# Kernel optimization log

Measured on AMD Instinct MI355X. Metric: run time of the kernel, lower is better.

## Reference

```python
import jax, jax.numpy as jnp
import numpy as np

NUM_CLASSES = 80
NUM_ANCHORS = 5
ANCHORS = np.array([1.3221, 1.73145, 3.19275, 4.00944, 5.05587, 8.09892,
                    9.47112, 4.84053, 11.2364, 10.0071], dtype=np.float32).reshape(NUM_ANCHORS, 2)
COORD_SCALE = 1.0
NOOBJECT_SCALE = 1.0
OBJECT_SCALE = 5.0
CLASS_SCALE = 1.0
SIL_THRESH = 0.6
MAX_T = 50  # max ground-truth boxes per image
NB, NH, NW = 32, 38, 38


def bbox_iou(b1, b2):
    """IoU for center-format boxes (..., 4) = (cx, cy, w, h); broadcastable.
    Matches darknet bbox_ious with x1y1x2y2=False (zero IoU if no overlap)."""
    mx = jnp.minimum(b1[..., 0] - b1[..., 2] / 2, b2[..., 0] - b2[..., 2] / 2)
    Mx = jnp.maximum(b1[..., 0] + b1[..., 2] / 2, b2[..., 0] + b2[..., 2] / 2)
    my = jnp.minimum(b1[..., 1] - b1[..., 3] / 2, b2[..., 1] - b2[..., 3] / 2)
    My = jnp.maximum(b1[..., 1] + b1[..., 3] / 2, b2[..., 1] + b2[..., 3] / 2)
    cw = b1[..., 2] + b2[..., 2] - (Mx - mx)
    ch = b1[..., 3] + b2[..., 3] - (My - my)
    inter = jnp.where((cw > 0) & (ch > 0), cw * ch, 0.0)
    union = b1[..., 2] * b1[..., 3] + b2[..., 2] * b2[..., 3] - inter
    return inter / jnp.maximum(union, 1e-12)


def setup_inputs() -> dict:
    key = jax.random.key(0)
    k1, k2, k3 = jax.random.split(key, 3)
    output = jax.random.normal(k1, (NB, NUM_ANCHORS * (5 + NUM_CLASSES), NH, NW), dtype=jnp.float32)
    # target rows: 50 boxes x (cls, x, y, w, h), normalized coords in (0,1)
    target = jax.random.uniform(k2, (NB, MAX_T * 5), dtype=jnp.float32, minval=0.02, maxval=0.98)
    features = jax.random.normal(k3, (NB, 512, NH, NW), dtype=jnp.float32)
    return {"output": output, "target": target, "features": features}


def _region_loss(output, target):
    nB, _, nH, nW = output.shape
    nA, nC = NUM_ANCHORS, NUM_CLASSES
    anchors = jnp.asarray(ANCHORS)
    sg = jax.lax.stop_gradient

    out5 = output.reshape(nB, nA, 5 + nC, nH, nW)
    x = jax.nn.sigmoid(out5[:, :, 0])
    y = jax.nn.sigmoid(out5[:, :, 1])
    w = out5[:, :, 2]
    h = out5[:, :, 3]
    conf = jax.nn.sigmoid(out5[:, :, 4])
    cls = jnp.transpose(out5[:, :, 5:], (0, 1, 3, 4, 2))  # [nB,nA,nH,nW,nC]

    # predicted boxes in grid units (detached, as pred_boxes uses .data in torch)
    grid_x = jnp.arange(nW, dtype=output.dtype)
    grid_y = jnp.arange(nH, dtype=output.dtype)
    px = sg(x) + grid_x[None, None, None, :]
    py = sg(y) + grid_y[None, None, :, None]
    pw = jnp.exp(sg(w)) * anchors[None, :, 0, None, None]
    ph = jnp.exp(sg(h)) * anchors[None, :, 1, None, None]
    pred_boxes = jnp.stack([px, py, pw, ph], axis=-1)  # [nB,nA,nH,nW,4]

    tgt = sg(target).reshape(nB, MAX_T, 5)
    gx = tgt[..., 1] * nW
    gy = tgt[..., 2] * nH
    gw = tgt[..., 3] * nW
    gh = tgt[..., 4] * nH
    # original loop breaks at first target x == 0 -> valid prefix mask
    valid = jnp.cumprod((tgt[..., 1] != 0).astype(jnp.int32), axis=1).astype(bool)

    # ---- conf_mask silencing: max IoU of every predicted box vs any GT ----
    gt_boxes = jnp.stack([gx, gy, gw, gh], axis=-1)  # [nB,50,4]
    pb_flat = pred_boxes.reshape(nB, 1, nA * nH * nW, 4)
    ious = bbox_iou(gt_boxes[:, :, None, :], pb_flat)  # [nB,50,nA*nH*nW]
    max_iou = jnp.where(valid[:, :, None], ious, 0.0).max(axis=1).reshape(nB, nA, nH, nW)
    conf_mask = jnp.where(max_iou > SIL_THRESH, 0.0, NOOBJECT_SCALE).astype(output.dtype)

    # ---- seen < 12800 warm-up branch (self.seen = 0, anchor_step = 2) ----
    shp = (nB, nA, nH, nW)
    tx = jnp.full(shp, 0.5, output.dtype)
    ty = jnp.full(shp, 0.5, output.dtype)
    tw = jnp.zeros(shp, output.dtype)
    th = jnp.zeros(shp, output.dtype)
    coord_mask = jnp.ones(shp, output.dtype)
    cls_mask = jnp.zeros(shp, output.dtype)
    tconf = jnp.zeros(shp, output.dtype)
    tcls = jnp.zeros(shp, jnp.int32)

    # ---- best anchor per GT (IoU of wh-only boxes; argmax keeps first max,
    #      matching the strict '>' update in the loop) ----
    zeros = jnp.zeros_like(gw)
    gt_wh = jnp.stack([zeros, zeros, gw, gh], axis=-1)[:, :, None, :]  # [nB,50,1,4]
    anc_wh = jnp.concatenate([jnp.zeros_like(anchors), anchors], axis=-1)[None, None]  # [1,1,nA,4]
    best_n = jnp.argmax(bbox_iou(gt_wh, anc_wh), axis=-1)  # [nB,50]

    gi = jnp.clip(jnp.floor(gx).astype(jnp.int32), 0, nW - 1)
    gj = jnp.clip(jnp.floor(gy).astype(jnp.int32), 0, nH - 1)

    b_idx = jnp.arange(nB)[:, None]
    pbox = pred_boxes[b_idx, best_n, gj, gi]  # [nB,50,4]
    iou_gt = bbox_iou(gt_boxes, pbox)  # [nB,50]

    tx_val = gx - gi.astype(output.dtype)
    ty_val = gy - gj.astype(output.dtype)
    tw_val = jnp.log(jnp.maximum(gw, 1e-12) / anchors[best_n, 0])
    th_val = jnp.log(jnp.maximum(gh, 1e-12) / anchors[best_n, 1])
    cls_val = tgt[..., 0].astype(jnp.int32)

    bi = jnp.arange(nB)

    def step(carry, t):
        coord_m, conf_m, cls_m, tx, ty, tw, th, tconf, tcls = carry
        bn = best_n[:, t]
        j = gj[:, t]
        i = gi[:, t]
        v = valid[:, t]

        def upd(arr, val):
            # indices are distinct within one step (one GT per batch element)
            old = arr[bi, bn, j, i]
            return arr.at[bi, bn, j, i].set(jnp.where(v, val, old))

        coord_m = upd(coord_m, 1.0)
        cls_m = upd(cls_m, 1.0)
        conf_m = upd(conf_m, OBJECT_SCALE)
        tx = upd(tx, tx_val[:, t])
        ty = upd(ty, ty_val[:, t])
        tw = upd(tw, tw_val[:, t])
        th = upd(th, th_val[:, t])
        tconf = upd(tconf, iou_gt[:, t])
        tcls = upd(tcls, cls_val[:, t])
        return (coord_m, conf_m, cls_m, tx, ty, tw, th, tconf, tcls), None

    init = (coord_mask, conf_mask, cls_mask, tx, ty, tw, th, tconf, tcls)
    (coord_mask, conf_mask, cls_mask, tx, ty, tw, th, tconf, tcls), _ = jax.lax.scan(
        step, init, jnp.arange(MAX_T))

    conf_mask = jnp.sqrt(conf_mask)

    loss_x = COORD_SCALE * jnp.sum((x * coord_mask - tx * coord_mask) ** 2) / 2.0
    loss_y = COORD_SCALE * jnp.sum((y * coord_mask - ty * coord_mask) ** 2) / 2.0
    loss_w = COORD_SCALE * jnp.sum((w * coord_mask - tw * coord_mask) ** 2) / 2.0
    loss_h = COORD_SCALE * jnp.sum((h * coord_mask - th * coord_mask) ** 2) / 2.0
    loss_conf = jnp.sum((conf * conf_mask - tconf * conf_mask) ** 2) / 2.0

    # sum-reduced cross entropy over cells where cls_mask == 1
    logp = jax.nn.log_softmax(cls, axis=-1)
    picked = jnp.take_along_axis(logp, tcls[..., None], axis=-1)[..., 0]
    loss_cls = -CLASS_SCALE * jnp.sum(cls_mask * picked)

    return loss_x + loss_y + loss_w + loss_h + loss_conf + loss_cls


def reference(output, target, features):
    # `features` feeds the truncated adversarial-defense tail of the original
    # forward; the detection region loss below is the complete surviving math.
    return _region_loss(output, target)
```

## Files before the change

### kernel.cpp

```cpp
#include <hip/hip_runtime.h>
#include <math.h>

#define NB 32
#define NA 5
#define NC 80
#define NH 38
#define NW 38
#define MAXT 50
#define CELLS (NH * NW)
#define CH (5 + NC)
#define REC_STRIDE 12
#define PREP_THREADS 256
#define NWAVES (PREP_THREADS / 64)

__device__ __forceinline__ float sigmoidf_(float v) {
    return 1.0f / (1.0f + expf(-v));
}

__device__ __forceinline__ float bbox_iou_(float ax, float ay, float aw, float ah,
                                           float bx, float by, float bw, float bh) {
    float mx = fminf(ax - aw * 0.5f, bx - bw * 0.5f);
    float Mx = fmaxf(ax + aw * 0.5f, bx + bw * 0.5f);
    float my = fminf(ay - ah * 0.5f, by - bh * 0.5f);
    float My = fmaxf(ay + ah * 0.5f, by + bh * 0.5f);
    float cw = aw + bw - (Mx - mx);
    float ch = ah + bh - (My - my);
    float inter = (cw > 0.0f && ch > 0.0f) ? cw * ch : 0.0f;
    float uni = aw * ah + bw * bh - inter;
    return inter / fmaxf(uni, 1e-12f);
}

__device__ __constant__ float c_anchors[10] = {
    1.3221f, 1.73145f, 3.19275f, 4.00944f, 5.05587f,
    8.09892f, 9.47112f, 4.84053f, 11.2364f, 10.0071f};

#define CLS_PART_OFF (NB * MAXT * REC_STRIDE)

__global__ void prep_gt_kernel(const float* __restrict__ out,
                               const float* __restrict__ tgt,
                               float* __restrict__ ws,
                               float* __restrict__ loss_out,
                               int out_size) {
    const int b = blockIdx.x;
    const int tid = threadIdx.x;
    const int wid = tid >> 6;
    const int lane = tid & 63;
    const int t = tid;

    if (b == 0) {
        for (int i = tid; i < out_size; i += PREP_THREADS) loss_out[i] = 0.0f;
    }

    __shared__ int s_nz[64];
    __shared__ int s_key[64];
    __shared__ int s_winner[MAXT];
    __shared__ int s_off[MAXT];
    __shared__ int s_cls[MAXT];
    __shared__ float s_cpart[NWAVES];

    float t0 = 0.f, t1 = 0.f, gx = 0.f, gy = 0.f, gw = 0.f, gh = 0.f;
    if (t < MAXT) {
        const float* tp = tgt + (long)b * (MAXT * 5) + t * 5;
        t0 = tp[0];
        t1 = tp[1];
        gx = t1 * NW;
        gy = tp[2] * NH;
        gw = tp[3] * NW;
        gh = tp[4] * NH;
    }
    if (t < 64) s_nz[t] = (t < MAXT) ? (t1 != 0.0f ? 1 : 0) : 1;
    __syncthreads();

    int key = -1;
    if (t < MAXT) {
        bool valid = true;
        for (int u = 0; u <= t; ++u)
            if (!s_nz[u]) { valid = false; break; }

        int bn = 0;
        float best = -1.0f;
        for (int a = 0; a < NA; ++a) {
            float aw = c_anchors[2 * a], ah = c_anchors[2 * a + 1];
            float inter = fminf(gw, aw) * fminf(gh, ah);
            float uni = gw * gh + aw * ah - inter;
            float iou = inter / fmaxf(uni, 1e-12f);
            if (iou > best) { best = iou; bn = a; }
        }
        int gi = (int)floorf(gx);
        gi = gi < 0 ? 0 : (gi > NW - 1 ? NW - 1 : gi);
        int gj = (int)floorf(gy);
        gj = gj < 0 ? 0 : (gj > NH - 1 ? NH - 1 : gj);

        long base = (((long)b * NA + bn) * CH) * CELLS + gj * NW + gi;
        float xr = out[base];
        float yr = out[base + CELLS];
        float wr = out[base + 2 * CELLS];
        float hr = out[base + 3 * CELLS];
        float px = sigmoidf_(xr) + (float)gi;
        float py = sigmoidf_(yr) + (float)gj;
        float pw = expf(wr) * c_anchors[2 * bn];
        float ph = expf(hr) * c_anchors[2 * bn + 1];
        float iou_gt = bbox_iou_(gx, gy, gw, gh, px, py, pw, ph);
        float txv = gx - (float)gi;
        float tyv = gy - (float)gj;
        float twv = logf(fmaxf(gw, 1e-12f) / c_anchors[2 * bn]);
        float thv = logf(fmaxf(gh, 1e-12f) / c_anchors[2 * bn + 1]);

        key = valid ? (bn * CELLS + gj * NW + gi) : -1;

        float* r = ws + ((long)b * MAXT + t) * REC_STRIDE;
        r[0] = gx; r[1] = gy; r[2] = gw; r[3] = gh;
        r[4] = valid ? 1.0f : 0.0f;
        r[5] = (float)key;
        r[6] = txv; r[7] = tyv; r[8] = twv; r[9] = thv;
        r[10] = iou_gt;
        r[11] = 0.0f;

        int cls = (int)t0;
        cls = cls < 0 ? 0 : (cls > NC - 1 ? NC - 1 : cls);
        s_cls[t] = cls;
        s_off[t] = (bn * CH + 5) * CELLS + gj * NW + gi;
    }
    if (t < 64) s_key[t] = key;
    __syncthreads();

    if (t < MAXT) {
        bool winner = (key >= 0);
        if (winner) {
            for (int u = t + 1; u < MAXT; ++u)
                if (s_key[u] == key) { winner = false; break; }
        }
        s_winner[t] = winner ? 1 : 0;
    }
    __syncthreads();

    const float* ob = out + (long)b * NA * CH * CELLS;
    float closs = 0.0f;
    for (int rt = wid; rt < MAXT; rt += NWAVES) {
        if (!s_winner[rt]) continue;
        const float* cp = ob + s_off[rt];
        float v0 = cp[(long)lane * CELLS];
        float v1 = (lane < NC - 64) ? cp[(long)(64 + lane) * CELLS] : -INFINITY;
        float m = fmaxf(v0, v1);
        for (int off = 32; off > 0; off >>= 1)
            m = fmaxf(m, __shfl_down(m, off));
        m = __shfl(m, 0);
        float e = expf(v0 - m) + ((lane < NC - 64) ? expf(v1 - m) : 0.0f);
        for (int off = 32; off > 0; off >>= 1)
            e += __shfl_down(e, off);
        if (lane == 0) {
            float lse = m + logf(e);
            closs += lse - cp[(long)s_cls[rt] * CELLS];
        }
    }
    if (lane == 0) s_cpart[wid] = closs;
    __syncthreads();
    if (tid == 0) {
        float s = 0.0f;
        for (int w = 0; w < NWAVES; ++w) s += s_cpart[w];
        ws[CLS_PART_OFF + b] = s;
    }
}

__global__ void cell_loss_kernel(const float* __restrict__ out,
                                 const float* __restrict__ ws,
                                 float* __restrict__ loss) {
    const int b = blockIdx.y;
    const int idx = blockIdx.x * blockDim.x + threadIdx.x;

    __shared__ float sr[MAXT][REC_STRIDE];
    for (int k = threadIdx.x; k < MAXT * REC_STRIDE; k += blockDim.x)
        ((float*)sr)[k] = ws[(long)b * MAXT * REC_STRIDE + k];
    __syncthreads();

    float cell = 0.0f;
    if (idx < NA * CELLS) {
        int a = idx / CELLS;
        int r = idx - a * CELLS;
        int j = r / NW;
        int i = r - j * NW;

        long base = (((long)b * NA + a) * CH) * CELLS + r;
        float xr = out[base];
        float yr = out[base + CELLS];
        float wr = out[base + 2 * CELLS];
        float hr = out[base + 3 * CELLS];
        float cr = out[base + 4 * CELLS];

        float sx = sigmoidf_(xr);
        float sy = sigmoidf_(yr);
        float sc = sigmoidf_(cr);
        float px = sx + (float)i;
        float py = sy + (float)j;
        float pw = expf(wr) * c_anchors[2 * a];
        float ph = expf(hr) * c_anchors[2 * a + 1];

        float mykey = (float)(a * CELLS + r);
        float max_iou = 0.0f;
        int m = -1;
        #pragma unroll 5
        for (int t = 0; t < MAXT; ++t) {
            if (sr[t][4] != 0.0f) {
                float iou = bbox_iou_(sr[t][0], sr[t][1], sr[t][2], sr[t][3],
                                      px, py, pw, ph);
                max_iou = fmaxf(max_iou, iou);
                if (sr[t][5] == mykey) m = t;
            }
        }

        float tx = 0.5f, ty = 0.5f, tw = 0.0f, th = 0.0f, tconf = 0.0f;
        float cscale = (max_iou > 0.6f) ? 0.0f : 1.0f;
        if (m >= 0) {
            tx = sr[m][6]; ty = sr[m][7]; tw = sr[m][8]; th = sr[m][9];
            tconf = sr[m][10];
            cscale = 5.0f;
        }
        float dx = sx - tx, dy = sy - ty, dw = wr - tw, dh = hr - th, dc = sc - tconf;
        cell = 0.5f * (dx * dx + dy * dy + dw * dw + dh * dh) + 0.5f * cscale * dc * dc;
    }

    float v = cell;
    for (int off = 32; off > 0; off >>= 1) v += __shfl_down(v, off);
    __shared__ float swave[4];
    int wid = threadIdx.x >> 6;
    int lane = threadIdx.x & 63;
    if (lane == 0) swave[wid] = v;
    __syncthreads();
    if (threadIdx.x == 0) {
        float s = swave[0] + swave[1] + swave[2] + swave[3];
        if (blockIdx.x == 0) s += ws[CLS_PART_OFF + b];
        atomicAdd(loss, s);
    }
}

extern "C" void kernel_launch(void* const* d_in, const int* in_sizes, int n_in,
                              void* d_out, int out_size, void* d_ws, size_t ws_size,
                              hipStream_t stream) {
    const float* output = (const float*)d_in[0];
    const float* target = (const float*)d_in[1];
    float* loss = (float*)d_out;
    float* ws = (float*)d_ws;

    prep_gt_kernel<<<NB, PREP_THREADS, 0, stream>>>(output, target, ws, loss, out_size);
    const int cells = NA * CELLS;
    dim3 grid((cells + 255) / 256, NB);
    cell_loss_kernel<<<grid, 256, 0, stream>>>(output, ws, loss);
}
```

Before: 206.2 us.

## Fuse GT prep and per-cell loss into one kernel with redundant per-block prep

Merges the ground-truth preparation kernel and the per-cell loss kernel into a single kernel launched over 8 slices per batch image. Each block recomputes the GT records in shared memory instead of passing them through a global workspace, then grid-strides over its slice of cells and shares the class-loss rows across slices. This removes the dependency between the two kernels and the workspace round trip. The cost is that GT prep is repeated 8 times per image, there is a separate tiny zeroing launch, and only 256 blocks are used instead of roughly 900.

```diff
diff --git a/kernel.cpp b/kernel.cpp
--- a/kernel.cpp
+++ b/kernel.cpp
@@ -9,9 +9,9 @@
 #define MAXT 50
 #define CELLS (NH * NW)
 #define CH (5 + NC)
-#define REC_STRIDE 12
-#define PREP_THREADS 256
-#define NWAVES (PREP_THREADS / 64)
+#define NSLICE 8
+#define THREADS 256
+#define NWAVES (THREADS / 64)
 
 __device__ __forceinline__ float sigmoidf_(float v) {
     return 1.0f / (1.0f + expf(-v));
@@ -34,29 +34,28 @@
     1.3221f, 1.73145f, 3.19275f, 4.00944f, 5.05587f,
     8.09892f, 9.47112f, 4.84053f, 11.2364f, 10.0071f};
 
-#define CLS_PART_OFF (NB * MAXT * REC_STRIDE)
-
-__global__ void prep_gt_kernel(const float* __restrict__ out,
-                               const float* __restrict__ tgt,
-                               float* __restrict__ ws,
-                               float* __restrict__ loss_out,
-                               int out_size) {
-    const int b = blockIdx.x;
+__global__ void zero_out_kernel(float* out, int n) {
+    int i = threadIdx.x;
+    if (i < n) out[i] = 0.0f;
+}
+
+__global__ void region_loss_kernel(const float* __restrict__ out,
+                                   const float* __restrict__ tgt,
+                                   float* __restrict__ loss) {
+    const int bx = blockIdx.x;
+    const int b = blockIdx.y;
     const int tid = threadIdx.x;
     const int wid = tid >> 6;
     const int lane = tid & 63;
     const int t = tid;
 
-    if (b == 0) {
-        for (int i = tid; i < out_size; i += PREP_THREADS) loss_out[i] = 0.0f;
-    }
-
     __shared__ int s_nz[64];
     __shared__ int s_key[64];
+    __shared__ float s_rec[MAXT][12];
     __shared__ int s_winner[MAXT];
     __shared__ int s_off[MAXT];
     __shared__ int s_cls[MAXT];
-    __shared__ float s_cpart[NWAVES];
+    __shared__ float s_wpart[NWAVES];
 
     float t0 = 0.f, t1 = 0.f, gx = 0.f, gy = 0.f, gw = 0.f, gh = 0.f;
     if (t < MAXT) {
@@ -101,20 +100,18 @@
         float pw = expf(wr) * c_anchors[2 * bn];
         float ph = expf(hr) * c_anchors[2 * bn + 1];
         float iou_gt = bbox_iou_(gx, gy, gw, gh, px, py, pw, ph);
-        float txv = gx - (float)gi;
-        float tyv = gy - (float)gj;
-        float twv = logf(fmaxf(gw, 1e-12f) / c_anchors[2 * bn]);
-        float thv = logf(fmaxf(gh, 1e-12f) / c_anchors[2 * bn + 1]);
 
         key = valid ? (bn * CELLS + gj * NW + gi) : -1;
 
-        float* r = ws + ((long)b * MAXT + t) * REC_STRIDE;
-        r[0] = gx; r[1] = gy; r[2] = gw; r[3] = gh;
-        r[4] = valid ? 1.0f : 0.0f;
-        r[5] = (float)key;
-        r[6] = txv; r[7] = tyv; r[8] = twv; r[9] = thv;
-        r[10] = iou_gt;
-        r[11] = 0.0f;
+        s_rec[t][0] = gx; s_rec[t][1] = gy; s_rec[t][2] = gw; s_rec[t][3] = gh;
+        s_rec[t][4] = valid ? 1.0f : 0.0f;
+        s_rec[t][5] = (float)key;
+        s_rec[t][6] = gx - (float)gi;
+        s_rec[t][7] = gy - (float)gj;
+        s_rec[t][8] = logf(fmaxf(gw, 1e-12f) / c_anchors[2 * bn]);
+        s_rec[t][9] = logf(fmaxf(gh, 1e-12f) / c_anchors[2 * bn + 1]);
+        s_rec[t][10] = iou_gt;
+        s_rec[t][11] = 0.0f;
 
         int cls = (int)t0;
         cls = cls < 0 ? 0 : (cls > NC - 1 ? NC - 1 : cls);
@@ -134,9 +131,57 @@
     }
     __syncthreads();
 
+    float cellsum = 0.0f;
+    for (int idx = bx * THREADS + tid; idx < NA * CELLS; idx += NSLICE * THREADS) {
+        int a = idx / CELLS;
+        int r = idx - a * CELLS;
+        int j = r / NW;
+        int i = r - j * NW;
+
+        long base = (((long)b * NA + a) * CH) * CELLS + r;
+        float xr = out[base];
+        float yr = out[base + CELLS];
+        float wr = out[base + 2 * CELLS];
+        float hr = out[base + 3 * CELLS];
+        float cr = out[base + 4 * CELLS];
+
+        float sx = sigmoidf_(xr);
+        float sy = sigmoidf_(yr);
+        float sc = sigmoidf_(cr);
+        float px = sx + (float)i;
+        float py = sy + (float)j;
+        float pw = expf(wr) * c_anchors[2 * a];
+        float ph = expf(hr) * c_anchors[2 * a + 1];
+
+        float mykey = (float)(a * CELLS + r);
+        float max_iou = 0.0f;
+        int m = -1;
+        #pragma unroll 5
+        for (int u = 0; u < MAXT; ++u) {
+            if (s_rec[u][4] != 0.0f) {
+                float iou = bbox_iou_(s_rec[u][0], s_rec[u][1], s_rec[u][2], s_rec[u][3],
+                                      px, py, pw, ph);
+                max_iou = fmaxf(max_iou, iou);
+                if (s_rec[u][5] == mykey) m = u;
+            }
+        }
+
+        float tx = 0.5f, ty = 0.5f, tw = 0.0f, th = 0.0f, tconf = 0.0f;
+        float cscale = (max_iou > 0.6f) ? 0.0f : 1.0f;
+        if (m >= 0) {
+            tx = s_rec[m][6]; ty = s_rec[m][7]; tw = s_rec[m][8]; th = s_rec[m][9];
+            tconf = s_rec[m][10];
+            cscale = 5.0f;
+        }
+        float dx = sx - tx, dy = sy - ty, dw = wr - tw, dh = hr - th, dc = sc - tconf;
+        cellsum += 0.5f * (dx * dx + dy * dy + dw * dw + dh * dh)
+                 + 0.5f * cscale * dc * dc;
+    }
+
     const float* ob = out + (long)b * NA * CH * CELLS;
+    const int gwave = bx * NWAVES + wid;
     float closs = 0.0f;
-    for (int rt = wid; rt < MAXT; rt += NWAVES) {
+    for (int rt = gwave; rt < MAXT; rt += NSLICE * NWAVES) {
         if (!s_winner[rt]) continue;
         const float* cp = ob + s_off[rt];
         float v0 = cp[(long)lane * CELLS];
@@ -153,82 +198,14 @@
             closs += lse - cp[(long)s_cls[rt] * CELLS];
         }
     }
-    if (lane == 0) s_cpart[wid] = closs;
+
+    float v = cellsum;
+    for (int off = 32; off > 0; off >>= 1) v += __shfl_down(v, off);
+    if (lane == 0) s_wpart[wid] = v + closs;
     __syncthreads();
     if (tid == 0) {
         float s = 0.0f;
-        for (int w = 0; w < NWAVES; ++w) s += s_cpart[w];
-        ws[CLS_PART_OFF + b] = s;
-    }
-}
-
-__global__ void cell_loss_kernel(const float* __restrict__ out,
-                                 const float* __restrict__ ws,
-                                 float* __restrict__ loss) {
-    const int b = blockIdx.y;
-    const int idx = blockIdx.x * blockDim.x + threadIdx.x;
-
-    __shared__ float sr[MAXT][REC_STRIDE];
-    for (int k = threadIdx.x; k < MAXT * REC_STRIDE; k += blockDim.x)
-        ((float*)sr)[k] = ws[(long)b * MAXT * REC_STRIDE + k];
-    __syncthreads();
-
-    float cell = 0.0f;
-    if (idx < NA * CELLS) {
-        int a = idx / CELLS;
-        int r = idx - a * CELLS;
-        int j = r / NW;
-        int i = r - j * NW;
-
-        long base = (((long)b * NA + a) * CH) * CELLS + r;
-        float xr = out[base];
-        float yr = out[base + CELLS];
-        float wr = out[base + 2 * CELLS];
-        float hr = out[base + 3 * CELLS];
-        float cr = out[base + 4 * CELLS];
-
-        float sx = sigmoidf_(xr);
-        float sy = sigmoidf_(yr);
-        float sc = sigmoidf_(cr);
-        float px = sx + (float)i;
-        float py = sy + (float)j;
-        float pw = expf(wr) * c_anchors[2 * a];
-        float ph = expf(hr) * c_anchors[2 * a + 1];
-
-        float mykey = (float)(a * CELLS + r);
-        float max_iou = 0.0f;
-        int m = -1;
-        #pragma unroll 5
-        for (int t = 0; t < MAXT; ++t) {
-            if (sr[t][4] != 0.0f) {
-                float iou = bbox_iou_(sr[t][0], sr[t][1], sr[t][2], sr[t][3],
-                                      px, py, pw, ph);
-                max_iou = fmaxf(max_iou, iou);
-                if (sr[t][5] == mykey) m = t;
-            }
-        }
-
-        float tx = 0.5f, ty = 0.5f, tw = 0.0f, th = 0.0f, tconf = 0.0f;
-        float cscale = (max_iou > 0.6f) ? 0.0f : 1.0f;
-        if (m >= 0) {
-            tx = sr[m][6]; ty = sr[m][7]; tw = sr[m][8]; th = sr[m][9];
-            tconf = sr[m][10];
-            cscale = 5.0f;
-        }
-        float dx = sx - tx, dy = sy - ty, dw = wr - tw, dh = hr - th, dc = sc - tconf;
-        cell = 0.5f * (dx * dx + dy * dy + dw * dw + dh * dh) + 0.5f * cscale * dc * dc;
-    }
-
-    float v = cell;
-    for (int off = 32; off > 0; off >>= 1) v += __shfl_down(v, off);
-    __shared__ float swave[4];
-    int wid = threadIdx.x >> 6;
-    int lane = threadIdx.x & 63;
-    if (lane == 0) swave[wid] = v;
-    __syncthreads();
-    if (threadIdx.x == 0) {
-        float s = swave[0] + swave[1] + swave[2] + swave[3];
-        if (blockIdx.x == 0) s += ws[CLS_PART_OFF + b];
+        for (int w = 0; w < NWAVES; ++w) s += s_wpart[w];
         atomicAdd(loss, s);
     }
 }
@@ -239,10 +216,8 @@
     const float* output = (const float*)d_in[0];
     const float* target = (const float*)d_in[1];
     float* loss = (float*)d_out;
-    float* ws = (float*)d_ws;
-
-    prep_gt_kernel<<<NB, PREP_THREADS, 0, stream>>>(output, target, ws, loss, out_size);
-    const int cells = NA * CELLS;
-    dim3 grid((cells + 255) / 256, NB);
-    cell_loss_kernel<<<grid, 256, 0, stream>>>(output, ws, loss);
-}
+
+    zero_out_kernel<<<1, 64, 0, stream>>>(loss, out_size);
+    dim3 grid(NSLICE, NB);
+    region_loss_kernel<<<grid, THREADS, 0, stream>>>(output, target, loss);
+}
```

After: 200.6 us. 2.7% less time.
